# Performance work log

Measured on AMD Instinct MI355X. Metric: run time of the kernel, lower is better.

Reference implementation:

```python
import jax, jax.numpy as jnp
import numpy as np

B, CIN, COUT, H, W = 2, 64, 64, 192, 192
G = 2          # offset groups (region + semantic offset branches concatenated)
KK = 9         # 3x3 kernel taps
CG = CIN // G  # channels per offset group


def conv2d(x, w, b):
    # NCHW, OIHW, stride 1, padding 1 (same as nn.Conv2d(k=3, s=1, p=1))
    y = jax.lax.conv_general_dilated(x, w, (1, 1), ((1, 1), (1, 1)),
                                     dimension_numbers=('NCHW', 'OIHW', 'NCHW'))
    return y + b[None, :, None, None]


def bilinear_gather(x, py, px):
    # x: (B,G,C,H,W); py,px: (B,G,K,H,W) absolute sample coords (float)
    b, g, c, h, w = x.shape
    k = py.shape[2]
    y0 = jnp.floor(py)
    x0 = jnp.floor(px)
    ly = (py - y0)[:, :, None]   # (B,G,1,K,H,W)
    lx = (px - x0)[:, :, None]
    xf = x.reshape(b, g, c, h * w)

    def corner(yi, xi):
        valid = (yi >= 0) & (yi < h) & (xi >= 0) & (xi < w)
        idx = (jnp.clip(yi, 0, h - 1).astype(jnp.int32) * w
               + jnp.clip(xi, 0, w - 1).astype(jnp.int32))          # (B,G,K,H,W)
        idxf = idx.reshape(b, g, k * h * w)
        gat = jax.vmap(jax.vmap(lambda xc, ic: jnp.take(xc, ic, axis=1)))(xf, idxf)
        gat = gat.reshape(b, g, c, k, h, w)
        return gat * valid[:, :, None].astype(x.dtype)

    v00 = corner(y0, x0)
    v01 = corner(y0, x0 + 1)
    v10 = corner(y0 + 1, x0)
    v11 = corner(y0 + 1, x0 + 1)
    return (v00 * (1 - ly) * (1 - lx) + v01 * (1 - ly) * lx
            + v10 * ly * (1 - lx) + v11 * ly * lx)


def setup_inputs() -> dict:
    key = jax.random.key(0)
    ks = jax.random.split(key, 12)
    stdv = 1.0 / np.sqrt(CIN * 9)
    inp = {
        'input': jax.random.normal(ks[0], (B, CIN, H, W), jnp.float32),
        'mask_in': jax.random.uniform(ks[1], (B, 1, H, W), jnp.float32),
        'weight': jax.random.uniform(ks[2], (COUT, CIN, 3, 3), jnp.float32, -stdv, stdv),
        'bias': jnp.zeros((COUT,), jnp.float32),
        'sem_w': jax.random.normal(ks[3], (2 * KK, CIN, 3, 3), jnp.float32) * 0.01,
        'sem_b': jnp.zeros((2 * KK,), jnp.float32),
        'reg_w': jax.random.normal(ks[4], (2 * KK, 1, 3, 3), jnp.float32) * 0.01,
        'reg_b': jnp.zeros((2 * KK,), jnp.float32),
        'm1_w': jax.random.normal(ks[5], (KK, 1, 3, 3), jnp.float32) * 0.1,
        'm1_b': jnp.zeros((KK,), jnp.float32),
        'm2_w': jax.random.normal(ks[6], (KK, CIN, 3, 3), jnp.float32) * 0.1,
        'm2_b': jnp.zeros((KK,), jnp.float32),
    }
    return inp


def reference(input, mask_in, weight, bias, sem_w, sem_b, reg_w, reg_b,
              m1_w, m1_b, m2_w, m2_b):
    f32 = input.dtype
    # --- learned offsets: region (group 0) then semantic (group 1) ---
    region_offset = conv2d(mask_in, reg_w, reg_b)    # (B, 2*9, H, W)
    semantic_offset = conv2d(input, sem_w, sem_b)    # (B, 2*9, H, W)
    offset = jnp.concatenate([region_offset, semantic_offset], axis=1)
    off = offset.reshape(B, G, KK, 2, H, W)          # [..., 0]=dy, [..., 1]=dx
    ky = (jnp.arange(KK) // 3 - 1).astype(f32)[None, None, :, None, None]
    kx = (jnp.arange(KK) % 3 - 1).astype(f32)[None, None, :, None, None]
    gy = jnp.arange(H, dtype=f32)[None, None, None, :, None]
    gx = jnp.arange(W, dtype=f32)[None, None, None, None, :]
    py = off[:, :, :, 0] + gy + ky                   # (B,G,K,H,W)
    px = off[:, :, :, 1] + gx + kx

    # --- update mask: deform conv of repeated mask with all-ones weight (no grad) ---
    # mask repeated over CIN channels -> identical within each offset group, so
    # sample one channel per group and scale: out = 2 (out chans) * CG * sum_{g,k}
    mgrp = jnp.broadcast_to(mask_in[:, None], (B, G, 1, H, W))
    sm = bilinear_gather(mgrp, py, px)               # (B,G,1,K,H,W)
    update_mask = jnp.clip(2.0 * CG * sm.sum(axis=(1, 2, 3)), 0.0, 1.0)[:, None]
    update_mask = jax.lax.stop_gradient(update_mask)  # (B,1,H,W)

    # --- modulation masks ---
    dm1 = jax.nn.sigmoid(conv2d(mask_in, m1_w, m1_b))  # (B,9,H,W) -> group 0
    dm2 = jax.nn.sigmoid(conv2d(input, m2_w, m2_b))    # (B,9,H,W) -> group 1
    dmask = jnp.concatenate([dm1, dm2], axis=1).reshape(B, G, KK, H, W)[:, :, None]

    # --- main modulated deformable conv ---
    xg = input.reshape(B, G, CG, H, W)
    sampled = bilinear_gather(xg, py, px) * dmask    # (B,G,CG,K,H,W)
    wr = weight.reshape(COUT, G, CG, KK)
    raw = jnp.einsum('bgckhw,ogck->bohw', sampled, wr) + bias[None, :, None, None]

    output = raw * update_mask
    return output, update_mask
```

## Files before the change

kernel.cpp:

```cpp
#include <hip/hip_runtime.h>
#include <hip/hip_fp16.h>
#include <math.h>

#define B_  2
#define CIN 64
#define COUT 64
#define H_  192
#define W_  192
#define G_  2
#define KK_ 9
#define CG_ 32
#define HW_ (H_*W_)
#define PIX 32
#define XT_ (W_/PIX)
#define PR_ 7
#define PC_ 38
#define PST 72
#define DSTR 69
#define RST 38
#define NB_NHWC (B_ * (HW_ / 64))
#define NB_WT   ((18*4*64*8 + 18*2*64*8) / 256)

typedef __attribute__((ext_vector_type(8))) short bf16x8;
typedef __attribute__((ext_vector_type(8))) _Float16 f16x8;
typedef __attribute__((ext_vector_type(4))) unsigned int u32x4;
typedef __attribute__((ext_vector_type(4))) float f32x4;

static __device__ __forceinline__ short f2h(float f) {
    _Float16 h = (_Float16)f;
    return __builtin_bit_cast(short, h);
}
static __device__ __forceinline__ float h2f(short s) {
    _Float16 h = __builtin_bit_cast(_Float16, s);
    return (float)h;
}
static __device__ __forceinline__ unsigned pk2hu(float lo, float hi) {
    auto h = __builtin_amdgcn_cvt_pkrtz(lo, hi);
    return __builtin_bit_cast(unsigned, h);
}
static __device__ __forceinline__ short2 pk2h(float lo, float hi) {
    auto h = __builtin_amdgcn_cvt_pkrtz(lo, hi);
    return __builtin_bit_cast(short2, h);
}
static __device__ __forceinline__ __half2 bcl(unsigned u) {
    return __builtin_bit_cast(__half2, (unsigned)((u & 0xffffu) | (u << 16)));
}
static __device__ __forceinline__ __half2 bch(unsigned u) {
    return __builtin_bit_cast(__half2, (unsigned)((u >> 16) | (u & 0xffff0000u)));
}
static __device__ __forceinline__ __half2 H2(unsigned u) {
    return __builtin_bit_cast(__half2, u);
}

__global__ __launch_bounds__(256)
void prep_kernel(const float* __restrict__ in,
                 const float* __restrict__ weight,
                 const float* __restrict__ sem_w,
                 const float* __restrict__ m2_w,
                 short* __restrict__ inpT,
                 short* __restrict__ wbm,
                 short* __restrict__ wbs) {
    __shared__ float t[64][65];
    const int tid = threadIdx.x;
    const int bid = blockIdx.x;
    if (bid < NB_NHWC) {
        const int b = bid / (HW_ / 64);
        const int pix0 = (bid % (HW_ / 64)) * 64;
        const float* src = in + (size_t)b * CIN * HW_ + pix0;
        const int c0 = (tid >> 6) * 16;
        const int p  = tid & 63;
        #pragma unroll
        for (int i = 0; i < 16; ++i)
            t[c0 + i][p] = src[(size_t)(c0 + i) * HW_ + p];
        __syncthreads();
        short* dst = inpT + ((size_t)b * HW_ + pix0) * 64;
        #pragma unroll
        for (int i = 0; i < 2; ++i) {
            int item = i * 256 + tid;
            int pp = item >> 3, oct = item & 7;
            bf16x8 v;
            #pragma unroll
            for (int j = 0; j < 8; j += 2) {
                short2 ss = pk2h(t[oct * 8 + j][pp], t[oct * 8 + j + 1][pp]);
                v[j] = ss.x; v[j + 1] = ss.y;
            }
            *(bf16x8*)&dst[pp * 64 + oct * 8] = v;
        }
        return;
    }
    int i = (bid - NB_NHWC) * 256 + tid;
    if (i < 18 * 4 * 64 * 8) {
        int j = i & 7, lane = (i >> 3) & 63, nt = (i >> 9) & 3, gk = i >> 11;
        int n = lane & 15, q = lane >> 4;
        int o = nt * 16 + n;
        int g = gk / 9, k = gk - g * 9;
        int cin = g * CG_ + q * 8 + j;
        wbm[i] = f2h(weight[(o * CIN + cin) * 9 + k]);
        return;
    }
    int ii = i - 18 * 4 * 64 * 8;
    if (ii >= 18 * 2 * 64 * 8) return;
    int j = ii & 7, lane = (ii >> 3) & 63, nt = (ii >> 9) & 1, s = ii >> 10;
    int t_ = s >> 1, h = s & 1;
    int n = lane & 15, q = lane >> 4;
    int o = nt * 16 + n;
    int c = h * 32 + q * 8 + j;
    float v = 0.f;
    if (o < 18)      v = sem_w[(o * CIN + c) * 9 + t_];
    else if (o < 27) v = m2_w[((o - 18) * CIN + c) * 9 + t_];
    wbs[ii] = f2h(v);
}

#define MSTEPP(GK, I0, I1) { \
    f16x8 wb0 = ((const f16x8*)wbm)[((GK) * 4 + 0) * 64 + lane]; \
    f16x8 wb1 = ((const f16x8*)wbm)[((GK) * 4 + 1) * 64 + lane]; \
    f16x8 wb2 = ((const f16x8*)wbm)[((GK) * 4 + 2) * 64 + lane]; \
    f16x8 wb3 = ((const f16x8*)wbm)[((GK) * 4 + 3) * 64 + lane]; \
    u32x4 d00 = *(const u32x4*)&pb[(I0)]; \
    u32x4 d01 = *(const u32x4*)&pb[(I0) + PST]; \
    u32x4 d10 = *(const u32x4*)&pb[(I0) + PC_ * PST]; \
    u32x4 d11 = *(const u32x4*)&pb[(I0) + (PC_ + 1) * PST]; \
    u32x4 e00 = *(const u32x4*)&pb[(I1)]; \
    u32x4 e01 = *(const u32x4*)&pb[(I1) + PST]; \
    u32x4 e10 = *(const u32x4*)&pb[(I1) + PC_ * PST]; \
    u32x4 e11 = *(const u32x4*)&pb[(I1) + (PC_ + 1) * PST]; \
    const uint2 mw0 = meta_w[(GK) * 32 + n]; \
    const uint2 mw1 = meta_w[(GK) * 32 + 16 + n]; \
    __half2 v00 = bcl(mw0.x), v01 = bch(mw0.x), v10 = bcl(mw0.y), v11 = bch(mw0.y); \
    __half2 u00 = bcl(mw1.x), u01 = bch(mw1.x), u10 = bcl(mw1.y), u11 = bch(mw1.y); \
    u32x4 ra, rb; \
    _Pragma("unroll") \
    for (int jj = 0; jj < 4; ++jj) { \
        __half2 s = __hfma2(H2(d00[jj]), v00, __hfma2(H2(d01[jj]), v01, \
                    __hfma2(H2(d10[jj]), v10, __hmul2(H2(d11[jj]), v11)))); \
        ra[jj] = __builtin_bit_cast(unsigned, s); \
        __half2 t = __hfma2(H2(e00[jj]), u00, __hfma2(H2(e01[jj]), u01, \
                    __hfma2(H2(e10[jj]), u10, __hmul2(H2(e11[jj]), u11)))); \
        rb[jj] = __builtin_bit_cast(unsigned, t); \
    } \
    f16x8 a0 = __builtin_bit_cast(f16x8, ra); \
    f16x8 a1 = __builtin_bit_cast(f16x8, rb); \
    ma00 = __builtin_amdgcn_mfma_f32_16x16x32_f16(a0, wb0, ma00, 0, 0, 0); \
    ma01 = __builtin_amdgcn_mfma_f32_16x16x32_f16(a0, wb1, ma01, 0, 0, 0); \
    ma02 = __builtin_amdgcn_mfma_f32_16x16x32_f16(a0, wb2, ma02, 0, 0, 0); \
    ma03 = __builtin_amdgcn_mfma_f32_16x16x32_f16(a0, wb3, ma03, 0, 0, 0); \
    ma10 = __builtin_amdgcn_mfma_f32_16x16x32_f16(a1, wb0, ma10, 0, 0, 0); \
    ma11 = __builtin_amdgcn_mfma_f32_16x16x32_f16(a1, wb1, ma11, 0, 0, 0); \
    ma12 = __builtin_amdgcn_mfma_f32_16x16x32_f16(a1, wb2, ma12, 0, 0, 0); \
    ma13 = __builtin_amdgcn_mfma_f32_16x16x32_f16(a1, wb3, ma13, 0, 0, 0); \
}

#define LIDX(GK, S) \
    const int i0_##S = (int)meta_i[(GK) * 32 + n] * PST; \
    const int i1_##S = (int)meta_i[(GK) * 32 + 16 + n] * PST;

#define UMRED { if (tid < 32) { \
    float s_ = ums[tid] + ums[32 + tid] + ums[64 + tid] + ums[96 + tid]; \
    float u_ = fminf(fmaxf(64.f * s_, 0.f), 1.f); \
    um_out[(size_t)b * HW_ + y * W_ + x0 + tid] = u_; \
    umv[tid] = u_; } }

#define DUMP() { \
    float* dw = dout + w * (32 * DSTR); \
    _Pragma("unroll") \
    for (int r = 0; r < 4; ++r) { \
        dw[(q * 4 + r) * DSTR +  0 + n] = ma00[r]; \
        dw[(q * 4 + r) * DSTR + 16 + n] = ma01[r]; \
        dw[(q * 4 + r) * DSTR + 32 + n] = ma02[r]; \
        dw[(q * 4 + r) * DSTR + 48 + n] = ma03[r]; \
        dw[(16 + q * 4 + r) * DSTR +  0 + n] = ma10[r]; \
        dw[(16 + q * 4 + r) * DSTR + 16 + n] = ma11[r]; \
        dw[(16 + q * 4 + r) * DSTR + 32 + n] = ma12[r]; \
        dw[(16 + q * 4 + r) * DSTR + 48 + n] = ma13[r]; \
    } \
}

#define COMPOFF(OL, OH, ML, MH) { \
    if (g == 0) { \
        _Pragma("unroll") for (int o = (OL); o < (OH); ++o) off_[o] = reg_b[o]; \
        _Pragma("unroll") for (int k = (ML); k < (MH); ++k) mm[k] = m1_b[k]; \
        _Pragma("unroll") for (int t = 0; t < 9; ++t) { \
            float vt = mv[t]; \
            _Pragma("unroll") for (int o = (OL); o < (OH); ++o) off_[o] += vt * reg_w[o * 9 + t]; \
            _Pragma("unroll") for (int k = (ML); k < (MH); ++k) mm[k] += vt * m1_w[k * 9 + t]; \
        } \
    } else { \
        _Pragma("unroll") for (int o = (OL); o < (OH); ++o) \
            off_[o] = h2f(redh[pxl * RST + o]) + h2f(redh[32 * RST + pxl * RST + o]) + sem_b[o]; \
        _Pragma("unroll") for (int k = (ML); k < (MH); ++k) \
            mm[k] = h2f(redh[pxl * RST + 18 + k]) + h2f(redh[32 * RST + pxl * RST + 18 + k]) + m2_b[k]; \
    } \
}

__global__ __launch_bounds__(256)
void fused_kernel(const short* __restrict__ inpT,
                  const float* __restrict__ mask_in,
                  const short* __restrict__ wbs,
                  const short* __restrict__ wbm,
                  const float* __restrict__ sem_b,
                  const float* __restrict__ reg_w, const float* __restrict__ reg_b,
                  const float* __restrict__ m1_w, const float* __restrict__ m1_b,
                  const float* __restrict__ m2_b,
                  const float* __restrict__ bias,
                  float* __restrict__ out, float* __restrict__ um_out) {
    __shared__ __align__(16) short patch[PR_ * PC_ * PST];
    __shared__ __align__(16) short redh[2 * 32 * RST];
    __shared__ __align__(8) uint2 meta_w[18 * 32];
    __shared__ unsigned short meta_i[18 * 32];
    __shared__ float ums[4 * 32];
    __shared__ float umv[32];
    float* dout = (float*)patch;

    const int tid  = threadIdx.x;
    const int lane = tid & 63;
    const int w    = __builtin_amdgcn_readfirstlane(tid >> 6);
    const int team = w >> 1;
    const int kh   = w & 1;
    const int n = lane & 15, q = lane >> 4;

    const int bid  = blockIdx.x;
    const int band = bid & 7;
    const int jb   = bid >> 3;
    const int xt   = jb % XT_;
    const int rr   = band * 48 + jb / XT_;
    const int y    = rr % H_;
    const int b    = rr / H_;
    const int x0   = xt * PIX;

    for (int i = tid; i < PR_ * PC_ * 8; i += 256) {
        int chunk = i & 7;
        int cc = (i >> 3) % PC_;
        int rp = (i >> 3) / PC_;
        int yy = y - 3 + rp;
        int xx = x0 - 3 + cc;
        bf16x8 v = {0, 0, 0, 0, 0, 0, 0, 0};
        if (yy >= 0 && yy < H_ && xx >= 0 && xx < W_)
            v = *(const bf16x8*)&inpT[((size_t)(b * HW_ + yy * W_ + xx)) * 64 + chunk * 8];
        *(bf16x8*)&patch[(rp * PC_ + cc) * PST + chunk * 8] = v;
    }
    __syncthreads();

    f32x4 acc0 = {0.f, 0.f, 0.f, 0.f}, acc1 = {0.f, 0.f, 0.f, 0.f};
    for (int ss = 0; ss < 9; ++ss) {
        int s = team * 9 + ss;
        int tt = s >> 1, hh = s & 1;
        int dy = tt / 3 - 1, dx = tt % 3 - 1;
        int r = dy + 3;
        int c = kh * 16 + n + dx + 3;
        f16x8 a = *(const f16x8*)&patch[(r * PC_ + c) * PST + hh * 32 + q * 8];
        f16x8 b0 = ((const f16x8*)wbs)[(s * 2 + 0) * 64 + lane];
        f16x8 b1 = ((const f16x8*)wbs)[(s * 2 + 1) * 64 + lane];
        acc0 = __builtin_amdgcn_mfma_f32_16x16x32_f16(a, b0, acc0, 0, 0, 0);
        acc1 = __builtin_amdgcn_mfma_f32_16x16x32_f16(a, b1, acc1, 0, 0, 0);
    }
    #pragma unroll
    for (int r = 0; r < 4; ++r) {
        redh[team * (32 * RST) + (kh * 16 + q * 4 + r) * RST + n]      = f2h(acc0[r]);
        redh[team * (32 * RST) + (kh * 16 + q * 4 + r) * RST + 16 + n] = f2h(acc1[r]);
    }
    __syncthreads();

    {
        const int g    = team;
        const int half = lane >> 5;
        const int pxl  = lane & 31;
        const int xl   = x0 + pxl;
        const int pixl = y * W_ + xl;
        const bool vxm = xl > 0, vxp = (xl + 1) < W_;
        const bool vym = y > 0,  vyp = (y + 1) < H_;
        const int qk = (kh << 1) | half;
        const int k0 = (qk == 0) ? 0 : (qk == 1) ? 3 : (qk == 2) ? 5 : 7;
        const int k1 = (qk == 0) ? 3 : (qk == 1) ? 5 : (qk == 2) ? 7 : 9;
        float off_[18], mm[9];
        float mv[9];
        if (g == 0) {
            const float* mbp = mask_in + (size_t)b * HW_ + pixl;
            mv[0] = (vym && vxm) ? mbp[-W_ - 1] : 0.f;
            mv[1] = vym ? mbp[-W_] : 0.f;
            mv[2] = (vym && vxp) ? mbp[-W_ + 1] : 0.f;
            mv[3] = vxm ? mbp[-1] : 0.f;
            mv[4] = mbp[0];
            mv[5] = vxp ? mbp[1] : 0.f;
            mv[6] = (vyp && vxm) ? mbp[W_ - 1] : 0.f;
            mv[7] = vyp ? mbp[W_] : 0.f;
            mv[8] = (vyp && vxp) ? mbp[W_ + 1] : 0.f;
        }
        if (kh == 0) { COMPOFF(0, 10, 0, 5) } else { COMPOFF(10, 18, 5, 9) }

        const float* mb = mask_in + (size_t)b * HW_;
        float s_um = 0.f;
        #pragma unroll
        for (int k = 0; k < 9; ++k) {
            if (k < k0 || k >= k1) continue;
            float Y = off_[2 * k]     + (float)y  + (float)(k / 3 - 1);
            float X = off_[2 * k + 1] + (float)xl + (float)(k % 3 - 1);
            int gk = g * 9 + k;
            float dm = 1.f / (1.f + __expf(-mm[k]));
            float y0f = floorf(Y), x0f = floorf(X);
            int yi0 = (int)y0f, xi0 = (int)x0f;
            float ly = Y - y0f, lx = X - x0f;
            int yi1 = yi0 + 1, xi1 = xi0 + 1;
            bool vy0 = (yi0 >= 0 && yi0 < H_), vy1 = (yi1 >= 0 && yi1 < H_);
            bool vx0 = (xi0 >= 0 && xi0 < W_), vx1 = (xi1 >= 0 && xi1 < W_);
            float w00f = (vy0 && vx0) ? (1.f - ly) * (1.f - lx) : 0.f;
            float w01f = (vy0 && vx1) ? (1.f - ly) * lx : 0.f;
            float w10f = (vy1 && vx0) ? ly * (1.f - lx) : 0.f;
            float w11f = (vy1 && vx1) ? ly * lx : 0.f;
            int yc0 = min(max(yi0, 0), H_ - 1), yc1 = min(max(yi1, 0), H_ - 1);
            int xc0 = min(max(xi0, 0), W_ - 1), xc1 = min(max(xi1, 0), W_ - 1);
            s_um += w00f * mb[yc0 * W_ + xc0] + w01f * mb[yc0 * W_ + xc1]
                  + w10f * mb[yc1 * W_ + xc0] + w11f * mb[yc1 * W_ + xc1];
            int r0 = min(max(yi0 - (y - 3), 0), PR_ - 2);
            int c0 = min(max(xi0 - (x0 - 3), 0), PC_ - 2);
            meta_w[gk * 32 + pxl] = make_uint2(pk2hu(w00f * dm, w01f * dm),
                                               pk2hu(w10f * dm, w11f * dm));
            meta_i[gk * 32 + pxl] = (unsigned short)(r0 * PC_ + c0);
        }
        s_um += __shfl_xor(s_um, 32);
        if (half == 0) ums[w * 32 + pxl] = s_um;
    }
    __syncthreads();

    f32x4 ma00 = {0.f,0.f,0.f,0.f}, ma01 = {0.f,0.f,0.f,0.f};
    f32x4 ma02 = {0.f,0.f,0.f,0.f}, ma03 = {0.f,0.f,0.f,0.f};
    f32x4 ma10 = {0.f,0.f,0.f,0.f}, ma11 = {0.f,0.f,0.f,0.f};
    f32x4 ma12 = {0.f,0.f,0.f,0.f}, ma13 = {0.f,0.f,0.f,0.f};
    {
        const short* pb = patch + team * 32 + q * 8;
        const int t9 = team * 9;
        if (kh == 0) {
            LIDX(t9 + 0, 0) LIDX(t9 + 1, 1) LIDX(t9 + 2, 2) LIDX(t9 + 3, 3) LIDX(t9 + 4, 4)
            UMRED
            MSTEPP(t9 + 0, i0_0, i1_0)
            MSTEPP(t9 + 1, i0_1, i1_1)
            MSTEPP(t9 + 2, i0_2, i1_2)
            MSTEPP(t9 + 3, i0_3, i1_3)
            MSTEPP(t9 + 4, i0_4, i1_4)
        } else {
            LIDX(t9 + 5, 0) LIDX(t9 + 6, 1) LIDX(t9 + 7, 2) LIDX(t9 + 8, 3)
            MSTEPP(t9 + 5, i0_0, i1_0)
            MSTEPP(t9 + 6, i0_1, i1_1)
            MSTEPP(t9 + 7, i0_2, i1_2)
            MSTEPP(t9 + 8, i0_3, i1_3)
        }
    }
    __syncthreads();

    DUMP();
    __syncthreads();

    {
        const int pxs = tid & 31;
        const int o0  = (tid >> 5) * 8;
        float u = umv[pxs];
        float* ob = out + ((size_t)b * COUT + o0) * HW_ + y * W_ + x0 + pxs;
        const float* bs = bias + o0;
        const float* dp = dout + pxs * DSTR + o0;
        #pragma unroll
        for (int o = 0; o < 8; ++o)
            ob[(size_t)o * HW_] = (dp[o] + dp[32 * DSTR + o] + dp[2 * 32 * DSTR + o]
                                   + dp[3 * 32 * DSTR + o] + bs[o]) * u;
    }
}

extern "C" void kernel_launch(void* const* d_in, const int* in_sizes, int n_in,
                              void* d_out, int out_size, void* d_ws, size_t ws_size,
                              hipStream_t stream) {
    const float* input   = (const float*)d_in[0];
    const float* mask_in = (const float*)d_in[1];
    const float* weight  = (const float*)d_in[2];
    const float* bias    = (const float*)d_in[3];
    const float* sem_w   = (const float*)d_in[4];
    const float* sem_b   = (const float*)d_in[5];
    const float* reg_w   = (const float*)d_in[6];
    const float* reg_b   = (const float*)d_in[7];
    const float* m1_w    = (const float*)d_in[8];
    const float* m1_b    = (const float*)d_in[9];
    const float* m2_w    = (const float*)d_in[10];
    const float* m2_b    = (const float*)d_in[11];

    float* out = (float*)d_out;
    float* um  = out + (size_t)B_ * COUT * HW_;

    short* inpT = (short*)d_ws;
    short* wbm  = inpT + (size_t)B_ * HW_ * 64;
    short* wbs  = wbm + 18 * 4 * 64 * 8;

    prep_kernel<<<NB_NHWC + NB_WT, 256, 0, stream>>>(
        input, weight, sem_w, m2_w, inpT, wbm, wbs);
    fused_kernel<<<B_ * H_ * XT_, 256, 0, stream>>>(
        inpT, mask_in, wbs, wbm, sem_b, reg_w, reg_b, m1_w, m1_b, m2_b,
        bias, out, um);
}
```

Baseline: 128.8 us.

## Split patch load to overlap halo rows with offset conv and prefetch weights

The input patch load is split in two. The three central rows needed by the 3x3 offset conv are loaded first, followed by a barrier. The remaining four halo rows are issued after that barrier, so their global loads overlap the offset-conv MFMAs. Offset-conv weights are preloaded into 18 registers before the loop, the first two main-conv weight steps are prefetched before the bilinear metadata phase, and launch bounds request 3 blocks per SM. This hides global load latency at the cost of more register pressure, which the occupancy hint may force into spills.

Result: no change. 128.3 us, median of 2 (-0.4%).

```diff
diff --git a/kernel.cpp b/kernel.cpp
--- a/kernel.cpp
+++ b/kernel.cpp
@@ -111,11 +111,7 @@
     wbs[ii] = f2h(v);
 }
 
-#define MSTEPP(GK, I0, I1) { \
-    f16x8 wb0 = ((const f16x8*)wbm)[((GK) * 4 + 0) * 64 + lane]; \
-    f16x8 wb1 = ((const f16x8*)wbm)[((GK) * 4 + 1) * 64 + lane]; \
-    f16x8 wb2 = ((const f16x8*)wbm)[((GK) * 4 + 2) * 64 + lane]; \
-    f16x8 wb3 = ((const f16x8*)wbm)[((GK) * 4 + 3) * 64 + lane]; \
+#define MBODY(GK, I0, I1, WB0, WB1, WB2, WB3) { \
     u32x4 d00 = *(const u32x4*)&pb[(I0)]; \
     u32x4 d01 = *(const u32x4*)&pb[(I0) + PST]; \
     u32x4 d10 = *(const u32x4*)&pb[(I0) + PC_ * PST]; \
@@ -140,14 +136,22 @@
     } \
     f16x8 a0 = __builtin_bit_cast(f16x8, ra); \
     f16x8 a1 = __builtin_bit_cast(f16x8, rb); \
-    ma00 = __builtin_amdgcn_mfma_f32_16x16x32_f16(a0, wb0, ma00, 0, 0, 0); \
-    ma01 = __builtin_amdgcn_mfma_f32_16x16x32_f16(a0, wb1, ma01, 0, 0, 0); \
-    ma02 = __builtin_amdgcn_mfma_f32_16x16x32_f16(a0, wb2, ma02, 0, 0, 0); \
-    ma03 = __builtin_amdgcn_mfma_f32_16x16x32_f16(a0, wb3, ma03, 0, 0, 0); \
-    ma10 = __builtin_amdgcn_mfma_f32_16x16x32_f16(a1, wb0, ma10, 0, 0, 0); \
-    ma11 = __builtin_amdgcn_mfma_f32_16x16x32_f16(a1, wb1, ma11, 0, 0, 0); \
-    ma12 = __builtin_amdgcn_mfma_f32_16x16x32_f16(a1, wb2, ma12, 0, 0, 0); \
-    ma13 = __builtin_amdgcn_mfma_f32_16x16x32_f16(a1, wb3, ma13, 0, 0, 0); \
+    ma00 = __builtin_amdgcn_mfma_f32_16x16x32_f16(a0, WB0, ma00, 0, 0, 0); \
+    ma01 = __builtin_amdgcn_mfma_f32_16x16x32_f16(a0, WB1, ma01, 0, 0, 0); \
+    ma02 = __builtin_amdgcn_mfma_f32_16x16x32_f16(a0, WB2, ma02, 0, 0, 0); \
+    ma03 = __builtin_amdgcn_mfma_f32_16x16x32_f16(a0, WB3, ma03, 0, 0, 0); \
+    ma10 = __builtin_amdgcn_mfma_f32_16x16x32_f16(a1, WB0, ma10, 0, 0, 0); \
+    ma11 = __builtin_amdgcn_mfma_f32_16x16x32_f16(a1, WB1, ma11, 0, 0, 0); \
+    ma12 = __builtin_amdgcn_mfma_f32_16x16x32_f16(a1, WB2, ma12, 0, 0, 0); \
+    ma13 = __builtin_amdgcn_mfma_f32_16x16x32_f16(a1, WB3, ma13, 0, 0, 0); \
+}
+
+#define MSTEPP(GK, I0, I1) { \
+    f16x8 wb0 = ((const f16x8*)wbm)[((GK) * 4 + 0) * 64 + lane]; \
+    f16x8 wb1 = ((const f16x8*)wbm)[((GK) * 4 + 1) * 64 + lane]; \
+    f16x8 wb2 = ((const f16x8*)wbm)[((GK) * 4 + 2) * 64 + lane]; \
+    f16x8 wb3 = ((const f16x8*)wbm)[((GK) * 4 + 3) * 64 + lane]; \
+    MBODY(GK, I0, I1, wb0, wb1, wb2, wb3) \
 }
 
 #define LIDX(GK, S) \
@@ -192,7 +196,7 @@
     } \
 }
 
-__global__ __launch_bounds__(256)
+__global__ __launch_bounds__(256, 3)
 void fused_kernel(const short* __restrict__ inpT,
                   const float* __restrict__ mask_in,
                   const short* __restrict__ wbs,
@@ -227,10 +231,18 @@
     const int b    = rr / H_;
     const int x0   = xt * PIX;
 
-    for (int i = tid; i < PR_ * PC_ * 8; i += 256) {
+    f16x8 wbsr[18];
+    #pragma unroll
+    for (int ss = 0; ss < 9; ++ss) {
+        int s = team * 9 + ss;
+        wbsr[ss * 2 + 0] = ((const f16x8*)wbs)[(s * 2 + 0) * 64 + lane];
+        wbsr[ss * 2 + 1] = ((const f16x8*)wbs)[(s * 2 + 1) * 64 + lane];
+    }
+
+    for (int i = tid; i < 3 * PC_ * 8; i += 256) {
         int chunk = i & 7;
         int cc = (i >> 3) % PC_;
-        int rp = (i >> 3) / PC_;
+        int rp = 2 + (i >> 3) / PC_;
         int yy = y - 3 + rp;
         int xx = x0 - 3 + cc;
         bf16x8 v = {0, 0, 0, 0, 0, 0, 0, 0};
@@ -240,7 +252,21 @@
     }
     __syncthreads();
 
+    for (int j = tid; j < 4 * PC_ * 8; j += 256) {
+        int chunk = j & 7;
+        int cc = (j >> 3) % PC_;
+        int rr4 = (j >> 3) / PC_;
+        int rp = rr4 + ((rr4 >= 2) ? 3 : 0);
+        int yy = y - 3 + rp;
+        int xx = x0 - 3 + cc;
+        bf16x8 v = {0, 0, 0, 0, 0, 0, 0, 0};
+        if (yy >= 0 && yy < H_ && xx >= 0 && xx < W_)
+            v = *(const bf16x8*)&inpT[((size_t)(b * HW_ + yy * W_ + xx)) * 64 + chunk * 8];
+        *(bf16x8*)&patch[(rp * PC_ + cc) * PST + chunk * 8] = v;
+    }
+
     f32x4 acc0 = {0.f, 0.f, 0.f, 0.f}, acc1 = {0.f, 0.f, 0.f, 0.f};
+    #pragma unroll
     for (int ss = 0; ss < 9; ++ss) {
         int s = team * 9 + ss;
         int tt = s >> 1, hh = s & 1;
@@ -248,10 +274,8 @@
         int r = dy + 3;
         int c = kh * 16 + n + dx + 3;
         f16x8 a = *(const f16x8*)&patch[(r * PC_ + c) * PST + hh * 32 + q * 8];
-        f16x8 b0 = ((const f16x8*)wbs)[(s * 2 + 0) * 64 + lane];
-        f16x8 b1 = ((const f16x8*)wbs)[(s * 2 + 1) * 64 + lane];
-        acc0 = __builtin_amdgcn_mfma_f32_16x16x32_f16(a, b0, acc0, 0, 0, 0);
-        acc1 = __builtin_amdgcn_mfma_f32_16x16x32_f16(a, b1, acc1, 0, 0, 0);
+        acc0 = __builtin_amdgcn_mfma_f32_16x16x32_f16(a, wbsr[ss * 2 + 0], acc0, 0, 0, 0);
+        acc1 = __builtin_amdgcn_mfma_f32_16x16x32_f16(a, wbsr[ss * 2 + 1], acc1, 0, 0, 0);
     }
     #pragma unroll
     for (int r = 0; r < 4; ++r) {
@@ -259,6 +283,19 @@
         redh[team * (32 * RST) + (kh * 16 + q * 4 + r) * RST + 16 + n] = f2h(acc1[r]);
     }
     __syncthreads();
+
+    f16x8 pw0, pw1, pw2, pw3, pw4, pw5, pw6, pw7;
+    {
+        const int gk0 = team * 9 + (kh ? 5 : 0);
+        pw0 = ((const f16x8*)wbm)[((gk0) * 4 + 0) * 64 + lane];
+        pw1 = ((const f16x8*)wbm)[((gk0) * 4 + 1) * 64 + lane];
+        pw2 = ((const f16x8*)wbm)[((gk0) * 4 + 2) * 64 + lane];
+        pw3 = ((const f16x8*)wbm)[((gk0) * 4 + 3) * 64 + lane];
+        pw4 = ((const f16x8*)wbm)[((gk0 + 1) * 4 + 0) * 64 + lane];
+        pw5 = ((const f16x8*)wbm)[((gk0 + 1) * 4 + 1) * 64 + lane];
+        pw6 = ((const f16x8*)wbm)[((gk0 + 1) * 4 + 2) * 64 + lane];
+        pw7 = ((const f16x8*)wbm)[((gk0 + 1) * 4 + 3) * 64 + lane];
+    }
 
     {
         const int g    = team;
@@ -331,15 +368,15 @@
         if (kh == 0) {
             LIDX(t9 + 0, 0) LIDX(t9 + 1, 1) LIDX(t9 + 2, 2) LIDX(t9 + 3, 3) LIDX(t9 + 4, 4)
             UMRED
-            MSTEPP(t9 + 0, i0_0, i1_0)
-            MSTEPP(t9 + 1, i0_1, i1_1)
+            MBODY(t9 + 0, i0_0, i1_0, pw0, pw1, pw2, pw3)
+            MBODY(t9 + 1, i0_1, i1_1, pw4, pw5, pw6, pw7)
             MSTEPP(t9 + 2, i0_2, i1_2)
             MSTEPP(t9 + 3, i0_3, i1_3)
             MSTEPP(t9 + 4, i0_4, i1_4)
         } else {
             LIDX(t9 + 5, 0) LIDX(t9 + 6, 1) LIDX(t9 + 7, 2) LIDX(t9 + 8, 3)
-            MSTEPP(t9 + 5, i0_0, i1_0)
-            MSTEPP(t9 + 6, i0_1, i1_1)
+            MBODY(t9 + 5, i0_0, i1_0, pw0, pw1, pw2, pw3)
+            MBODY(t9 + 6, i0_1, i1_1, pw4, pw5, pw6, pw7)
             MSTEPP(t9 + 7, i0_2, i1_2)
             MSTEPP(t9 + 8, i0_3, i1_3)
         }
```
